# Optimization experiments

Hardware: AMD Instinct MI355X
Metric: run time of the kernel (lower is better)

## Reference

```python
import jax, jax.numpy as jnp
import numpy as np

B, S, H, V, C = 32, 512, 256, 50000, 5
NUM_LAYERS, WINDOW = 2, 2


def setup_inputs() -> dict:
    key = jax.random.key(0)
    ks = jax.random.split(key, 24)
    std = 0.1  # matches nn.init.normal_(p, 0, 0.1)
    n = lambda k, shp: jax.random.normal(k, shp, dtype=jnp.float32) * std
    u = lambda k, shp: -0.05 + jax.random.uniform(k, shp, dtype=jnp.float32) * 0.1
    return {
        "input_sentences": jax.random.randint(ks[0], (B, S), 0, V),
        "sentences_length": jax.random.randint(ks[1], (B,), 1, S),
        "hh0": u(ks[2], (B, S, H)),
        "cs0": u(ks[3], (B, S, H)),
        "embed": n(ks[4], (V, H)),
        # stacked word-gate weights, gate order: i, l, r, f, s, output, u
        "W_lr": n(ks[5], (7, H, 2 * H)),
        "W_c": n(ks[6], (7, H, H)),
        "W_x": n(ks[7], (7, H, H)),
        "W_g": n(ks[8], (7, H, H)),
        "gate_bias": n(ks[9], (7, H)),
        # sentence-state gates
        "W_fg_g": n(ks[10], (H, H)),
        "W_fg_h": n(ks[11], (H, H)),
        "W_fgi_g": n(ks[12], (H, H)),
        "W_fgi_h": n(ks[13], (H, H)),
        "W_og_g": n(ks[14], (H, H)),
        "W_og_h": n(ks[15], (H, H)),
        "b_fg": n(ks[16], (H,)),
        "b_fgi": n(ks[17], (H,)),
        # output head
        "W1": n(ks[18], (H, 2 * H)),
        "b1": n(ks[19], (H,)),
        "Wout": n(ks[20], (C, H)),
        "bout": n(ks[21], (C,)),
    }


def _before_sum(x, window):
    # sum of right-shifted (zero-padded at front) copies, shifts 1..window
    out = jnp.zeros_like(x)
    for s in range(1, window + 1):
        out = out + jnp.pad(x[:, :-s], ((0, 0), (s, 0), (0, 0)))
    return out


def _after_sum(x, window):
    out = jnp.zeros_like(x)
    for s in range(1, window + 1):
        out = out + jnp.pad(x[:, s:], ((0, 0), (0, s), (0, 0)))
    return out


def _slstm_step(hh, cs, sv, scs, wv, W_lr, W_c, W_x, W_g, gate_bias,
                W_fg_g, W_fg_h, W_fgi_g, W_fgi_h, W_og_g, W_og_h, b_fg, b_fgi):
    avg_hh = hh.mean(axis=1)                                   # [B,H]
    f_hat_g = jax.nn.sigmoid(sv @ W_fg_g.T + avg_hh @ W_fg_h.T + b_fg)
    # NOTE: original code (faithfully) uses output_gate_bias here, not output_gate_g_bias
    og_g = jax.nn.sigmoid(sv @ W_og_g.T + avg_hh @ W_og_h.T + gate_bias[5])
    f_hat_g_i = jax.nn.sigmoid((sv @ W_fgi_g.T)[:, None] + hh @ W_fgi_h.T + b_fgi)
    scores = jax.nn.softmax(f_hat_g_i, axis=2)                 # over hidden dim
    new_scs = jax.nn.softmax(f_hat_g, axis=1) * scs + (scores * cs).sum(axis=1)
    new_sv = og_g * jnp.tanh(new_scs)

    hb = _before_sum(hh, WINDOW)
    ha = _after_sum(hh, WINDOW)
    cb = _before_sum(cs, WINDOW)
    ca = _after_sum(cs, WINDOW)
    ba = jnp.concatenate([hb, ha], axis=-1)                    # [B,S,2H]

    # all 7 gate pre-activations at once: [B,S,7,H]
    pre = (jnp.einsum('bsk,ghk->bsgh', ba, W_lr)
           + jnp.einsum('bsk,ghk->bsgh', hh, W_c)
           + jnp.einsum('bsk,ghk->bsgh', wv, W_x)
           + (jnp.einsum('bk,ghk->bgh', new_sv, W_g) + gate_bias)[:, None])

    g5 = jax.nn.sigmoid(pre[..., :5, :])                       # i,l,r,f,s
    b_, s_ = g5.shape[:2]
    # joint softmax over the concatenated 5*H gate vector (as in torch cat+softmax)
    g5 = jax.nn.softmax(g5.reshape(b_, s_, -1), axis=-1).reshape(b_, s_, 5, -1)
    i_t, l_t, r_t, f_t, s_t = (g5[..., k, :] for k in range(5))
    og = jax.nn.sigmoid(pre[..., 5, :])
    u_g = jnp.tanh(pre[..., 6, :])

    new_cs = l_t * cb + f_t * cs + r_t * ca + s_t * scs[:, None] + i_t * u_g
    new_hh = og * jnp.tanh(new_cs)
    return new_hh, new_cs, new_sv, new_scs


def reference(input_sentences, sentences_length, hh0, cs0, embed,
              W_lr, W_c, W_x, W_g, gate_bias,
              W_fg_g, W_fg_h, W_fgi_g, W_fgi_h, W_og_g, W_og_h, b_fg, b_fgi,
              W1, b1, Wout, bout):
    wv = embed[input_sentences]                                # [B,S,H]
    hh, cs = hh0, cs0
    sv, scs = hh0.mean(axis=1), cs0.mean(axis=1)
    for _ in range(NUM_LAYERS):
        hh, cs, sv, scs = _slstm_step(hh, cs, sv, scs, wv,
                                      W_lr, W_c, W_x, W_g, gate_bias,
                                      W_fg_g, W_fg_h, W_fgi_g, W_fgi_h,
                                      W_og_g, W_og_h, b_fg, b_fgi)
    avg_hh = hh.mean(axis=1)
    conc = jnp.concatenate([avg_hh, sv], axis=1) @ W1.T + b1
    fc = conc @ Wout.T + bout
    return jax.nn.log_softmax(fc, axis=1), sv
```

## Files before the change

kernel.cpp:

```cpp
#include <hip/hip_runtime.h>
#include <stdint.h>
#include <math.h>

#define B_   32
#define S_   512
#define H_   256
#define M_   (B_*S_)
#define KBIG 1024
#define NB   1792
#define NB2  2048
#define C_   5

typedef __bf16 bf16;
typedef __bf16 bf16x4 __attribute__((ext_vector_type(4)));
typedef __bf16 bf16x8 __attribute__((ext_vector_type(8)));
typedef float  floatx4 __attribute__((ext_vector_type(4)));

__device__ __forceinline__ float sigm(float x){ return 1.f/(1.f+expf(-x)); }

__device__ __forceinline__ void gl16(const bf16* g, bf16* l){
    __builtin_amdgcn_global_load_lds(
        (const __attribute__((address_space(1))) unsigned int*)g,
        (__attribute__((address_space(3))) unsigned int*)l, 16, 0, 0);
}

__global__ void wcomb_k(const float* __restrict__ Wlr, const float* __restrict__ Wc,
                        const float* __restrict__ Wx, const float* __restrict__ Wfgi,
                        bf16* __restrict__ WT){
    int n = blockIdx.x;
    int k4 = threadIdx.x * 4;
    float4 v;
    if (n < NB){
        int g = n >> 8, h = n & 255;
        const float* src;
        if (k4 < 512)      src = Wlr + ((size_t)(g*256 + h))*512 + k4;
        else if (k4 < 768) src = Wc  + ((size_t)(g*256 + h))*256 + (k4 - 512);
        else               src = Wx  + ((size_t)(g*256 + h))*256 + (k4 - 768);
        v = *(const float4*)src;
    } else {
        int h = n - NB;
        if (k4 >= 512 && k4 < 768) v = *(const float4*)(Wfgi + (size_t)h*H_ + (k4 - 512));
        else { v.x=0.f; v.y=0.f; v.z=0.f; v.w=0.f; }
    }
    bf16 o[4] = {(bf16)v.x,(bf16)v.y,(bf16)v.z,(bf16)v.w};
    *(uint2*)&WT[(size_t)n*KBIG + k4] = *(uint2*)o;
}

__global__ void gather_k(const int* __restrict__ idx, const float* __restrict__ embed,
                         bf16* __restrict__ X){
    int i4 = (blockIdx.x*256 + threadIdx.x)*4;
    int m = i4 >> 8, h = i4 & 255;
    float4 v = *(const float4*)(embed + (size_t)idx[m]*H_ + h);
    bf16 o[4] = {(bf16)v.x,(bf16)v.y,(bf16)v.z,(bf16)v.w};
    *(uint2*)(X + (size_t)m*KBIG + 768 + h) = *(uint2*)o;
}

__global__ void mean1_k(const float* __restrict__ x, float* __restrict__ part){
    int b = blockIdx.x, c = blockIdx.y, h = threadIdx.x;
    const float* p = x + ((size_t)b*S_ + c*32)*H_ + h;
    float s = 0.f;
    #pragma unroll 8
    for (int t=0;t<32;t++) s += p[(size_t)t*H_];
    part[((size_t)b*16 + c)*H_ + h] = s;
}
__global__ void mean2_k(const float* __restrict__ part, float* __restrict__ out){
    int b = blockIdx.x, h = threadIdx.x;
    float s = 0.f;
    #pragma unroll
    for (int c=0;c<16;c++) s += part[((size_t)b*16 + c)*H_ + h];
    out[b*H_ + h] = s * (1.f/512.f);
}

__global__ void buildx_k(const float* __restrict__ hh, bf16* __restrict__ X){
    int m = blockIdx.x, tid = threadIdx.x;
    int seg = tid >> 6, li = tid & 63;
    int s = m & (S_-1);
    int h0 = li*4;
    size_t base = (size_t)m*H_ + h0;
    bf16* xr = X + (size_t)m*KBIG + seg*H_ + h0;
    const float4 z = {0.f,0.f,0.f,0.f};
    float4 v;
    if (seg == 0){
        float4 a = (s>=1) ? *(const float4*)&hh[base - H_]   : z;
        float4 b = (s>=2) ? *(const float4*)&hh[base - 2*H_] : z;
        v.x=a.x+b.x; v.y=a.y+b.y; v.z=a.z+b.z; v.w=a.w+b.w;
    } else if (seg == 1){
        float4 a = (s<=S_-2) ? *(const float4*)&hh[base + H_]   : z;
        float4 b = (s<=S_-3) ? *(const float4*)&hh[base + 2*H_] : z;
        v.x=a.x+b.x; v.y=a.y+b.y; v.z=a.z+b.z; v.w=a.w+b.w;
    } else {
        v = *(const float4*)&hh[base];
    }
    bf16 o[4] = {(bf16)v.x,(bf16)v.y,(bf16)v.z,(bf16)v.w};
    *(uint2*)xr = *(uint2*)o;
}

__global__ void mv5_k(const float* __restrict__ sv, const float* __restrict__ avg,
    const float* __restrict__ Wfg_g, const float* __restrict__ Wfg_h,
    const float* __restrict__ Wog_g, const float* __restrict__ Wog_h,
    const float* __restrict__ Wfgi_g, float* __restrict__ res){
    int j = blockIdx.x, b = blockIdx.y, h = threadIdx.x;
    const float* vec = (j==1 || j==3) ? avg + b*H_ : sv + b*H_;
    const float* W   = (j==0)?Wfg_g:(j==1)?Wfg_h:(j==2)?Wog_g:(j==3)?Wog_h:Wfgi_g;
    __shared__ float v[H_];
    v[h] = vec[h]; __syncthreads();
    const float* w = W + (size_t)h*H_;
    float d = 0.f;
    for (int k=0;k<H_;k++) d += v[k]*w[k];
    res[((size_t)b*5 + j)*H_ + h] = d;
}
__global__ void comb_k(const float* __restrict__ res, const float* __restrict__ b_fg,
                       const float* __restrict__ gbias, const float* __restrict__ b_fgi,
                       float* __restrict__ fhg, float* __restrict__ ogg,
                       float* __restrict__ svg){
    int b = blockIdx.x, h = threadIdx.x;
    const float* r = res + (size_t)b*5*H_;
    fhg[b*H_+h] = sigm(r[h] + r[H_+h] + b_fg[h]);
    ogg[b*H_+h] = sigm(r[2*H_+h] + r[3*H_+h] + gbias[5*H_+h]);
    svg[b*H_+h] = r[4*H_+h] + b_fgi[h];
}

__device__ __forceinline__ void mmq(floatx4 (&acc)[8][4], bf16x8 (&af)[4][2], bf16x8 (&bfr)[2][2],
                                    int MH, int NH){
    #pragma unroll
    for (int mi2=0;mi2<4;mi2++)
        #pragma unroll
        for (int ni2=0;ni2<2;ni2++)
            #pragma unroll
            for (int kk=0;kk<2;kk++)
                acc[MH*4+mi2][NH*2+ni2] = __builtin_amdgcn_mfma_f32_16x16x32_bf16(
                    af[mi2][kk], bfr[ni2][kk], acc[MH*4+mi2][NH*2+ni2], 0, 0, 0);
}

__global__ __launch_bounds__(512, 2)
void mgemm256_k(const bf16* __restrict__ A, const bf16* __restrict__ BT,
                bf16* __restrict__ C, int Kdim, int lda, int ldb, int ldc, int nbx){
    __shared__ alignas(16) bf16 lsA[2][256*64];
    __shared__ alignas(16) bf16 lsB[2][256*64];
    const int tid  = threadIdx.x;
    const int lane = tid & 63;
    const int wave = tid >> 6;
    const int wm = wave >> 2;
    const int wn = wave & 3;
    const int lrow = lane & 15, quad = lane >> 4;

    const int cpx = gridDim.x >> 3;
    const int w   = (blockIdx.x & 7)*cpx + (blockIdx.x >> 3);
    const int mb  = w / nbx, nb = w - mb*nbx;
    const int m0 = mb * 256, n0 = nb * 256;

    const int srow = tid >> 3;
    const int scol = ((tid & 7) ^ (srow & 7)) * 8;
    const bf16* Ab = A  + (size_t)(m0 + srow)*lda + scol;
    const bf16* Bb = BT + (size_t)(n0 + srow)*ldb + scol;
    const int NT = Kdim >> 6;

    floatx4 zero = {0.f,0.f,0.f,0.f};
    floatx4 acc[8][4];
    #pragma unroll
    for (int i=0;i<8;i++)
        #pragma unroll
        for (int j=0;j<4;j++) acc[i][j] = zero;
    bf16x8 af[4][2], bfrA[2][2], bfrB[2][2];

#define SA_(bu,r,kt) gl16(Ab + (size_t)(r)*64*lda + (size_t)(kt)*64, &lsA[bu][(r)*4096 + tid*8])
#define SB_(bu,r,kt) gl16(Bb + (size_t)(r)*64*ldb + (size_t)(kt)*64, &lsB[bu][(r)*4096 + tid*8])
#define RA_(bu,MH,mi2,kk) (*(const bf16x8*)&lsA[bu][(wm*128 + (MH)*64 + (mi2)*16 + lrow)*64 + ((((kk)*4+quad) ^ (lrow&7))*8)])
#define RB_(bu,NH,ni2,kk) (*(const bf16x8*)&lsB[bu][(wn*64  + (NH)*32 + (ni2)*16 + lrow)*64 + ((((kk)*4+quad) ^ (lrow&7))*8)])

    SB_(0,0,0); SB_(0,1,0); SB_(0,2,0); SB_(0,3,0);
    SA_(0,0,0); SA_(0,2,0); SA_(0,1,0); SA_(0,3,0);
    asm volatile("s_waitcnt vmcnt(2)" ::: "memory");
    __builtin_amdgcn_s_barrier();

    for (int kt = 0; kt < NT; ++kt){
        const int cur = kt & 1, nxt = cur ^ 1;
        const bool st = (kt + 1 < NT);
        const int k1 = kt + 1;

        #pragma unroll
        for (int mi2=0;mi2<4;mi2++){ af[mi2][0] = RA_(cur,0,mi2,0); af[mi2][1] = RA_(cur,0,mi2,1); }
        #pragma unroll
        for (int ni2=0;ni2<2;ni2++){ bfrA[ni2][0] = RB_(cur,0,ni2,0); bfrA[ni2][1] = RB_(cur,0,ni2,1); }
        if (st){ SB_(nxt,0,k1); SB_(nxt,1,k1); }
        __builtin_amdgcn_s_barrier();
        __builtin_amdgcn_s_setprio(1);
        mmq(acc, af, bfrA, 0, 0);
        __builtin_amdgcn_s_setprio(0);
        __builtin_amdgcn_s_barrier();

        #pragma unroll
        for (int ni2=0;ni2<2;ni2++){ bfrB[ni2][0] = RB_(cur,1,ni2,0); bfrB[ni2][1] = RB_(cur,1,ni2,1); }
        if (st){ SB_(nxt,2,k1); SB_(nxt,3,k1); }
        __builtin_amdgcn_s_barrier();
        __builtin_amdgcn_s_setprio(1);
        mmq(acc, af, bfrB, 0, 1);
        __builtin_amdgcn_s_setprio(0);
        if (st) asm volatile("s_waitcnt vmcnt(4)" ::: "memory");
        else    asm volatile("s_waitcnt vmcnt(0)" ::: "memory");
        __builtin_amdgcn_s_barrier();

        #pragma unroll
        for (int mi2=0;mi2<4;mi2++){ af[mi2][0] = RA_(cur,1,mi2,0); af[mi2][1] = RA_(cur,1,mi2,1); }
        if (st){ SA_(nxt,0,k1); SA_(nxt,2,k1); }
        __builtin_amdgcn_s_barrier();
        __builtin_amdgcn_s_setprio(1);
        mmq(acc, af, bfrB, 1, 1);
        __builtin_amdgcn_s_setprio(0);
        __builtin_amdgcn_s_barrier();

        if (st){ SA_(nxt,1,k1); SA_(nxt,3,k1); }
        __builtin_amdgcn_s_barrier();
        __builtin_amdgcn_s_setprio(1);
        mmq(acc, af, bfrA, 1, 0);
        __builtin_amdgcn_s_setprio(0);
        if (st) asm volatile("s_waitcnt vmcnt(2)" ::: "memory");
        __builtin_amdgcn_s_barrier();
    }
#undef SA_
#undef SB_
#undef RA_
#undef RB_

    #pragma unroll
    for (int mi=0;mi<8;mi++)
        #pragma unroll
        for (int ni=0;ni<4;ni++){
            int row = m0 + wm*128 + mi*16 + quad*4;
            int col = n0 + wn*64  + ni*16 + lrow;
            #pragma unroll
            for (int r=0;r<4;r++)
                C[(size_t)(row+r)*ldc + col] = (bf16)acc[mi][ni][r];
        }
}

__global__ void scorep_k(const bf16* __restrict__ fgih, const float* __restrict__ svg,
                         const float* __restrict__ cs, float* __restrict__ part, int ldf){
    int chunk = blockIdx.x, b = blockIdx.y;
    int tid = threadIdx.x, wave = tid >> 6, lane = tid & 63;
    __shared__ float acc4[4][256];
    int h0 = lane*4;
    float4 swv = *(const float4*)&svg[b*H_ + h0];
    float sw[4] = {swv.x, swv.y, swv.z, swv.w};
    float acc[4] = {0.f,0.f,0.f,0.f};
    for (int t=wave; t<16; t+=4){
        int m = b*S_ + chunk*16 + t;
        bf16x4 fv = *(const bf16x4*)&fgih[(size_t)m*ldf + h0];
        float e[4], loc = 0.f;
        #pragma unroll
        for (int j=0;j<4;j++){ e[j] = expf(sigm(sw[j] + (float)fv[j])); loc += e[j]; }
        #pragma unroll
        for (int off=32; off; off>>=1) loc += __shfl_xor(loc, off, 64);
        float inv = 1.f/loc;
        float4 cv = *(const float4*)&cs[(size_t)m*H_ + h0];
        acc[0] += e[0]*inv*cv.x; acc[1] += e[1]*inv*cv.y;
        acc[2] += e[2]*inv*cv.z; acc[3] += e[3]*inv*cv.w;
    }
    #pragma unroll
    for (int j=0;j<4;j++) acc4[wave][h0+j] = acc[j];
    __syncthreads();
    part[((size_t)b*32 + chunk)*H_ + tid] =
        acc4[0][tid] + acc4[1][tid] + acc4[2][tid] + acc4[3][tid];
}

__global__ void newscs_k(const float* __restrict__ part, const float* __restrict__ fhg,
                         const float* __restrict__ ogg, const float* __restrict__ scs_in,
                         float* __restrict__ scs_out, float* __restrict__ sv_out){
    int b = blockIdx.x, h = threadIdx.x;
    __shared__ float r[256];
    float dot = 0.f;
    #pragma unroll 8
    for (int c=0;c<32;c++) dot += part[((size_t)b*32+c)*H_ + h];
    float e = expf(fhg[b*H_+h]);
    r[h] = e; __syncthreads();
    for (int off=128; off; off>>=1){ if (h<off) r[h] += r[h+off]; __syncthreads(); }
    float ns = (e / r[0]) * scs_in[b*H_+h] + dot;
    scs_out[b*H_+h] = ns;
    sv_out[b*H_+h]  = ogg[b*H_+h] * tanhf(ns);
}

__global__ void gterm_k(const float* __restrict__ svn, const float* __restrict__ Wg,
                        const float* __restrict__ gbias, float* __restrict__ gt){
    int g = blockIdx.x, b = blockIdx.y, h = threadIdx.x;
    __shared__ float s[H_];
    s[h] = svn[b*H_+h]; __syncthreads();
    const float* w = Wg + ((size_t)g*H_ + h)*H_;
    float d = 0.f;
    for (int k=0;k<H_;k++) d += s[k]*w[k];
    gt[(size_t)b*NB + g*H_ + h] = d + gbias[g*H_+h];
}

__global__ void gates_k(const bf16* __restrict__ pre, const float* __restrict__ gt,
                        const float* __restrict__ cs_in, const float* __restrict__ scs_in,
                        float* __restrict__ hh_out, float* __restrict__ cs_out,
                        bf16* __restrict__ Xn, int ldp){
    int tid = threadIdx.x, wave = tid >> 6, lane = tid & 63;
    int m = blockIdx.x*4 + wave;
    int b = m >> 9, s = m & (S_-1);
    const bf16* row = pre + (size_t)m*ldp;
    int h0 = lane*4;
    float pv[7][4];
    #pragma unroll
    for (int g=0; g<7; ++g){
        bf16x4 t = *(const bf16x4*)&row[g*H_ + h0];
        float4 gq = *(const float4*)&gt[(size_t)b*NB + g*H_ + h0];
        pv[g][0] = (float)t[0] + gq.x;
        pv[g][1] = (float)t[1] + gq.y;
        pv[g][2] = (float)t[2] + gq.z;
        pv[g][3] = (float)t[3] + gq.w;
    }
    float ex[5][4], og[4], u[4];
    float loc = 0.f;
    #pragma unroll
    for (int g=0; g<5; ++g)
        #pragma unroll
        for (int j=0;j<4;j++){ float e = expf(sigm(pv[g][j])); ex[g][j] = e; loc += e; }
    #pragma unroll
    for (int j=0;j<4;j++){ og[j] = sigm(pv[5][j]); u[j] = tanhf(pv[6][j]); }
    #pragma unroll
    for (int off=32; off; off>>=1) loc += __shfl_xor(loc, off, 64);
    float inv = 1.f / loc;

    size_t i0 = (size_t)m*H_ + h0;
    const float4 z = {0.f,0.f,0.f,0.f};
    float4 c0  = *(const float4*)&cs_in[i0];
    float4 cm1 = (s>=1)    ? *(const float4*)&cs_in[i0 - H_]   : z;
    float4 cm2 = (s>=2)    ? *(const float4*)&cs_in[i0 - 2*H_] : z;
    float4 cp1 = (s<=S_-2) ? *(const float4*)&cs_in[i0 + H_]   : z;
    float4 cp2 = (s<=S_-3) ? *(const float4*)&cs_in[i0 + 2*H_] : z;
    float4 sc  = *(const float4*)&scs_in[(size_t)b*H_ + h0];
    float4 nc4, nh4;
    #pragma unroll
    for (int j=0;j<4;j++){
        float cb = ((const float*)&cm1)[j] + ((const float*)&cm2)[j];
        float ca = ((const float*)&cp1)[j] + ((const float*)&cp2)[j];
        float nc = ex[1][j]*inv*cb + ex[3][j]*inv*((const float*)&c0)[j] + ex[2][j]*inv*ca
                 + ex[4][j]*inv*((const float*)&sc)[j] + ex[0][j]*inv*u[j];
        ((float*)&nc4)[j] = nc;
        ((float*)&nh4)[j] = og[j] * tanhf(nc);
    }
    *(float4*)&cs_out[i0] = nc4;
    *(float4*)&hh_out[i0] = nh4;
    if (Xn){
        bf16 o[4] = {(bf16)((float*)&nh4)[0], (bf16)((float*)&nh4)[1],
                     (bf16)((float*)&nh4)[2], (bf16)((float*)&nh4)[3]};
        *(uint2*)&Xn[(size_t)m*KBIG + 512 + h0] = *(uint2*)o;
    }
}

__global__ void head_k(const float* __restrict__ avgh, const float* __restrict__ sv,
                       const float* __restrict__ W1, const float* __restrict__ b1,
                       const float* __restrict__ Wout, const float* __restrict__ bout,
                       float* __restrict__ out){
    int b = blockIdx.x, t = threadIdx.x;
    __shared__ float conc[H_];
    __shared__ float fc[8];
    const float* wr = W1 + (size_t)t*512;
    float d = b1[t];
    for (int k=0;k<H_;k++) d += avgh[b*H_+k]*wr[k];
    for (int k=0;k<H_;k++) d += sv[b*H_+k]*wr[256+k];
    conc[t] = d;
    __syncthreads();
    if (t < C_){
        const float* wo = Wout + (size_t)t*H_;
        float s = bout[t];
        for (int i=0;i<H_;i++) s += conc[i]*wo[i];
        fc[t] = s;
    }
    __syncthreads();
    if (t == 0){
        float mx = fc[0];
        for (int c=1;c<C_;c++) mx = fmaxf(mx, fc[c]);
        float se = 0.f;
        for (int c=0;c<C_;c++) se += expf(fc[c]-mx);
        float lse = mx + logf(se);
        for (int c=0;c<C_;c++) out[b*C_+c] = fc[c]-lse;
    }
    out[B_*C_ + b*H_ + t] = sv[b*H_+t];
}

extern "C" void kernel_launch(void* const* d_in, const int* in_sizes, int n_in,
                              void* d_out, int out_size, void* d_ws, size_t ws_size,
                              hipStream_t stream){
    const int*   idx    = (const int*)d_in[0];
    const float* hh0    = (const float*)d_in[2];
    const float* cs0    = (const float*)d_in[3];
    const float* embed  = (const float*)d_in[4];
    const float* Wlr    = (const float*)d_in[5];
    const float* Wc     = (const float*)d_in[6];
    const float* Wx     = (const float*)d_in[7];
    const float* Wg     = (const float*)d_in[8];
    const float* gbias  = (const float*)d_in[9];
    const float* Wfg_g  = (const float*)d_in[10];
    const float* Wfg_h  = (const float*)d_in[11];
    const float* Wfgi_g = (const float*)d_in[12];
    const float* Wfgi_h = (const float*)d_in[13];
    const float* Wog_g  = (const float*)d_in[14];
    const float* Wog_h  = (const float*)d_in[15];
    const float* b_fg   = (const float*)d_in[16];
    const float* b_fgi  = (const float*)d_in[17];
    const float* W1     = (const float*)d_in[18];
    const float* b1     = (const float*)d_in[19];
    const float* Wout   = (const float*)d_in[20];
    const float* bout   = (const float*)d_in[21];

    uint8_t* p = (uint8_t*)d_ws;
    auto alloc = [&](size_t bytes)->void*{ void* r=(void*)p; p += (bytes + 255) & ~(size_t)255; return r; };
    bf16*  WT    = (bf16*)alloc((size_t)NB2*KBIG*2);
    bf16*  X     = (bf16*)alloc((size_t)M_*KBIG*2);
    bf16*  pre   = (bf16*)alloc((size_t)M_*NB2*2);
    float* hhA = (float*)alloc((size_t)M_*H_*4);
    float* csA = (float*)alloc((size_t)M_*H_*4);
    float* hhB = (float*)alloc((size_t)M_*H_*4);
    float* csB = (float*)alloc((size_t)M_*H_*4);
    float* mpart= (float*)alloc((size_t)B_*16*H_*4);
    float* part = (float*)alloc((size_t)B_*32*H_*4);
    float* res5 = (float*)alloc((size_t)B_*5*H_*4);
    float* avgh = (float*)alloc(B_*H_*4);
    float* fhg  = (float*)alloc(B_*H_*4);
    float* ogg  = (float*)alloc(B_*H_*4);
    float* svg  = (float*)alloc(B_*H_*4);
    float* svP0 = (float*)alloc(B_*H_*4);
    float* svP1 = (float*)alloc(B_*H_*4);
    float* scP0 = (float*)alloc(B_*H_*4);
    float* scP1 = (float*)alloc(B_*H_*4);
    float* gt   = (float*)alloc((size_t)B_*NB*4);

    wcomb_k <<<NB2,         256, 0, stream>>>(Wlr, Wc, Wx, Wfgi_h, WT);
    gather_k<<<(M_*H_)/1024,256, 0, stream>>>(idx, embed, X);
    mean1_k <<<dim3(B_,16), 256, 0, stream>>>(hh0, mpart);
    mean2_k <<<B_,          256, 0, stream>>>(mpart, svP0);
    mean1_k <<<dim3(B_,16), 256, 0, stream>>>(cs0, mpart);
    mean2_k <<<B_,          256, 0, stream>>>(mpart, scP0);

    const float *hin = hh0, *cin = cs0;
    float *hout = hhA, *cout = csA;
    float *svin = svP0, *scin = scP0, *svout = svP1, *scout = scP1;

    for (int l=0; l<2; ++l){
        const float* avgp;
        if (l == 0){
            avgp = svin;
        } else {
            mean1_k<<<dim3(B_,16), 256, 0, stream>>>(hin, mpart);
            mean2_k<<<B_,          256, 0, stream>>>(mpart, avgh);
            avgp = avgh;
        }
        mv5_k   <<<dim3(5,B_), 256, 0, stream>>>(svin, avgp, Wfg_g, Wfg_h, Wog_g,
                                                 Wog_h, Wfgi_g, res5);
        comb_k  <<<B_, 256, 0, stream>>>(res5, b_fg, gbias, b_fgi, fhg, ogg, svg);
        buildx_k<<<M_, (l==0 ? 192 : 128), 0, stream>>>(hin, X);
        mgemm256_k<<<512, 512, 0, stream>>>(X, WT, pre, KBIG, KBIG, KBIG, NB2, 8);
        scorep_k<<<dim3(32,B_), 256, 0, stream>>>(pre + NB, svg, cin, part, NB2);
        newscs_k<<<B_, 256, 0, stream>>>(part, fhg, ogg, scin, scout, svout);
        gterm_k <<<dim3(7,B_), 256, 0, stream>>>(svout, Wg, gbias, gt);
        gates_k <<<M_/4, 256, 0, stream>>>(pre, gt, cin, scin, hout, cout,
                                           (l==0 ? X : (bf16*)nullptr), NB2);
        hin = hout; cin = cout;
        hout = (l==0) ? hhB : hhA;
        cout = (l==0) ? csB : csA;
        float* q;
        q = svin; svin = svout; svout = q;
        q = scin; scin = scout; scout = q;
    }
    mean1_k<<<dim3(B_,16), 256, 0, stream>>>(hin, mpart);
    mean2_k<<<B_,          256, 0, stream>>>(mpart, avgh);
    head_k <<<B_, 256, 0, stream>>>(avgh, svin, W1, b1, Wout, bout, (float*)d_out);
}
```

Before: 515.4 us.

## Fold comb kernel into consumers, vectorize matvec loops, remap block indices

Removes the comb_k launch and recomputes its sigmoid and bias terms directly inside scorep_k and newscs_k from res5. The small matrix-vector kernels (mv5, gterm, head) now read weights as float4 with unrolled loops, and the head stages its input vectors in shared memory. buildx_k and gates_k get a block-index swizzle that spreads consecutive blocks across distant rows, likely to balance memory channels or XCDs. The work per call is unchanged, but some gate math is now repeated across blocks and the remapping changes cache locality.

Result: no change. 512.0 us (-0.7%).

```diff
diff --git a/kernel.cpp b/kernel.cpp
--- a/kernel.cpp
+++ b/kernel.cpp
@@ -72,7 +72,9 @@
 }
 
 __global__ void buildx_k(const float* __restrict__ hh, bf16* __restrict__ X){
-    int m = blockIdx.x, tid = threadIdx.x;
+    int bid = blockIdx.x;
+    int m = (bid & 7)*(M_/8) + (bid >> 3);
+    int tid = threadIdx.x;
     int seg = tid >> 6, li = tid & 63;
     int s = m & (S_-1);
     int h0 = li*4;
@@ -106,18 +108,13 @@
     v[h] = vec[h]; __syncthreads();
     const float* w = W + (size_t)h*H_;
     float d = 0.f;
-    for (int k=0;k<H_;k++) d += v[k]*w[k];
+    #pragma unroll 4
+    for (int k=0;k<H_;k+=4){
+        float4 wv4 = *(const float4*)&w[k];
+        float4 vv4 = *(const float4*)&v[k];
+        d += vv4.x*wv4.x + vv4.y*wv4.y + vv4.z*wv4.z + vv4.w*wv4.w;
+    }
     res[((size_t)b*5 + j)*H_ + h] = d;
-}
-__global__ void comb_k(const float* __restrict__ res, const float* __restrict__ b_fg,
-                       const float* __restrict__ gbias, const float* __restrict__ b_fgi,
-                       float* __restrict__ fhg, float* __restrict__ ogg,
-                       float* __restrict__ svg){
-    int b = blockIdx.x, h = threadIdx.x;
-    const float* r = res + (size_t)b*5*H_;
-    fhg[b*H_+h] = sigm(r[h] + r[H_+h] + b_fg[h]);
-    ogg[b*H_+h] = sigm(r[2*H_+h] + r[3*H_+h] + gbias[5*H_+h]);
-    svg[b*H_+h] = r[4*H_+h] + b_fgi[h];
 }
 
 __device__ __forceinline__ void mmq(floatx4 (&acc)[8][4], bf16x8 (&af)[4][2], bf16x8 (&bfr)[2][2],
@@ -234,14 +231,16 @@
         }
 }
 
-__global__ void scorep_k(const bf16* __restrict__ fgih, const float* __restrict__ svg,
+__global__ void scorep_k(const bf16* __restrict__ fgih, const float* __restrict__ res5,
+                         const float* __restrict__ b_fgi,
                          const float* __restrict__ cs, float* __restrict__ part, int ldf){
     int chunk = blockIdx.x, b = blockIdx.y;
     int tid = threadIdx.x, wave = tid >> 6, lane = tid & 63;
     __shared__ float acc4[4][256];
     int h0 = lane*4;
-    float4 swv = *(const float4*)&svg[b*H_ + h0];
-    float sw[4] = {swv.x, swv.y, swv.z, swv.w};
+    float4 r4 = *(const float4*)&res5[((size_t)b*5 + 4)*H_ + h0];
+    float4 bf = *(const float4*)&b_fgi[h0];
+    float sw[4] = {r4.x+bf.x, r4.y+bf.y, r4.z+bf.z, r4.w+bf.w};
     float acc[4] = {0.f,0.f,0.f,0.f};
     for (int t=wave; t<16; t+=4){
         int m = b*S_ + chunk*16 + t;
@@ -263,20 +262,24 @@
         acc4[0][tid] + acc4[1][tid] + acc4[2][tid] + acc4[3][tid];
 }
 
-__global__ void newscs_k(const float* __restrict__ part, const float* __restrict__ fhg,
-                         const float* __restrict__ ogg, const float* __restrict__ scs_in,
+__global__ void newscs_k(const float* __restrict__ part, const float* __restrict__ res5,
+                         const float* __restrict__ b_fg, const float* __restrict__ gbias,
+                         const float* __restrict__ scs_in,
                          float* __restrict__ scs_out, float* __restrict__ sv_out){
     int b = blockIdx.x, h = threadIdx.x;
     __shared__ float r[256];
     float dot = 0.f;
     #pragma unroll 8
     for (int c=0;c<32;c++) dot += part[((size_t)b*32+c)*H_ + h];
-    float e = expf(fhg[b*H_+h]);
+    const float* rr = res5 + (size_t)b*5*H_;
+    float fhg = sigm(rr[h] + rr[H_+h] + b_fg[h]);
+    float ogg = sigm(rr[2*H_+h] + rr[3*H_+h] + gbias[5*H_+h]);
+    float e = expf(fhg);
     r[h] = e; __syncthreads();
     for (int off=128; off; off>>=1){ if (h<off) r[h] += r[h+off]; __syncthreads(); }
     float ns = (e / r[0]) * scs_in[b*H_+h] + dot;
     scs_out[b*H_+h] = ns;
-    sv_out[b*H_+h]  = ogg[b*H_+h] * tanhf(ns);
+    sv_out[b*H_+h]  = ogg * tanhf(ns);
 }
 
 __global__ void gterm_k(const float* __restrict__ svn, const float* __restrict__ Wg,
@@ -286,7 +289,12 @@
     s[h] = svn[b*H_+h]; __syncthreads();
     const float* w = Wg + ((size_t)g*H_ + h)*H_;
     float d = 0.f;
-    for (int k=0;k<H_;k++) d += s[k]*w[k];
+    #pragma unroll 4
+    for (int k=0;k<H_;k+=4){
+        float4 wv4 = *(const float4*)&w[k];
+        float4 vv4 = *(const float4*)&s[k];
+        d += vv4.x*wv4.x + vv4.y*wv4.y + vv4.z*wv4.z + vv4.w*wv4.w;
+    }
     gt[(size_t)b*NB + g*H_ + h] = d + gbias[g*H_+h];
 }
 
@@ -295,7 +303,9 @@
                         float* __restrict__ hh_out, float* __restrict__ cs_out,
                         bf16* __restrict__ Xn, int ldp){
     int tid = threadIdx.x, wave = tid >> 6, lane = tid & 63;
-    int m = blockIdx.x*4 + wave;
+    int bid = blockIdx.x;
+    int bid2 = (bid & 7)*(M_/32) + (bid >> 3);
+    int m = bid2*4 + wave;
     int b = m >> 9, s = m & (S_-1);
     const bf16* row = pre + (size_t)m*ldp;
     int h0 = lane*4;
@@ -353,18 +363,36 @@
                        const float* __restrict__ Wout, const float* __restrict__ bout,
                        float* __restrict__ out){
     int b = blockIdx.x, t = threadIdx.x;
+    __shared__ float sa[H_], ss[H_];
     __shared__ float conc[H_];
     __shared__ float fc[8];
+    sa[t] = avgh[b*H_+t]; ss[t] = sv[b*H_+t];
+    __syncthreads();
     const float* wr = W1 + (size_t)t*512;
     float d = b1[t];
-    for (int k=0;k<H_;k++) d += avgh[b*H_+k]*wr[k];
-    for (int k=0;k<H_;k++) d += sv[b*H_+k]*wr[256+k];
+    #pragma unroll 4
+    for (int k=0;k<H_;k+=4){
+        float4 w4 = *(const float4*)&wr[k];
+        float4 a4 = *(const float4*)&sa[k];
+        d += a4.x*w4.x + a4.y*w4.y + a4.z*w4.z + a4.w*w4.w;
+    }
+    #pragma unroll 4
+    for (int k=0;k<H_;k+=4){
+        float4 w4 = *(const float4*)&wr[256+k];
+        float4 s4 = *(const float4*)&ss[k];
+        d += s4.x*w4.x + s4.y*w4.y + s4.z*w4.z + s4.w*w4.w;
+    }
     conc[t] = d;
     __syncthreads();
     if (t < C_){
         const float* wo = Wout + (size_t)t*H_;
         float s = bout[t];
-        for (int i=0;i<H_;i++) s += conc[i]*wo[i];
+        #pragma unroll 4
+        for (int i=0;i<H_;i+=4){
+            float4 w4 = *(const float4*)&wo[i];
+            float4 c4 = *(const float4*)&conc[i];
+            s += c4.x*w4.x + c4.y*w4.y + c4.z*w4.z + c4.w*w4.w;
+        }
         fc[t] = s;
     }
     __syncthreads();
@@ -376,7 +404,7 @@
         float lse = mx + logf(se);
         for (int c=0;c<C_;c++) out[b*C_+c] = fc[c]-lse;
     }
-    out[B_*C_ + b*H_ + t] = sv[b*H_+t];
+    out[B_*C_ + b*H_ + t] = ss[t];
 }
 
 extern "C" void kernel_launch(void* const* d_in, const int* in_sizes, int n_in,
@@ -417,9 +445,6 @@
     float* part = (float*)alloc((size_t)B_*32*H_*4);
     float* res5 = (float*)alloc((size_t)B_*5*H_*4);
     float* avgh = (float*)alloc(B_*H_*4);
-    float* fhg  = (float*)alloc(B_*H_*4);
-    float* ogg  = (float*)alloc(B_*H_*4);
-    float* svg  = (float*)alloc(B_*H_*4);
     float* svP0 = (float*)alloc(B_*H_*4);
     float* svP1 = (float*)alloc(B_*H_*4);
     float* scP0 = (float*)alloc(B_*H_*4);
@@ -448,11 +473,10 @@
         }
         mv5_k   <<<dim3(5,B_), 256, 0, stream>>>(svin, avgp, Wfg_g, Wfg_h, Wog_g,
                                                  Wog_h, Wfgi_g, res5);
-        comb_k  <<<B_, 256, 0, stream>>>(res5, b_fg, gbias, b_fgi, fhg, ogg, svg);
         buildx_k<<<M_, (l==0 ? 192 : 128), 0, stream>>>(hin, X);
         mgemm256_k<<<512, 512, 0, stream>>>(X, WT, pre, KBIG, KBIG, KBIG, NB2, 8);
-        scorep_k<<<dim3(32,B_), 256, 0, stream>>>(pre + NB, svg, cin, part, NB2);
-        newscs_k<<<B_, 256, 0, stream>>>(part, fhg, ogg, scin, scout, svout);
+        scorep_k<<<dim3(32,B_), 256, 0, stream>>>(pre + NB, res5, b_fgi, cin, part, NB2);
+        newscs_k<<<B_, 256, 0, stream>>>(part, res5, b_fg, gbias, scin, scout, svout);
         gterm_k <<<dim3(7,B_), 256, 0, stream>>>(svout, Wg, gbias, gt);
         gates_k <<<M_/4, 256, 0, stream>>>(pre, gt, cin, scin, hout, cout,
                                            (l==0 ? X : (bf16*)nullptr), NB2);
```
